# Performance work log

Hardware: AMD Instinct MI355X
Metric: run time of the kernel (lower is better)

Reference implementation:

```python
import jax, jax.numpy as jnp
import numpy as np

EPS_BN = 1e-5
EPS_LN = 1e-5


def conv2d(x, w, stride=1, padding=0):
    # x: [B,C,H,W], w: [O,I,kh,kw]
    return jax.lax.conv_general_dilated(
        x, w, (stride, stride), [(padding, padding), (padding, padding)],
        dimension_numbers=("NCHW", "OIHW", "NCHW"))


def bn_relu(x, g, b, m, v):
    inv = g / jnp.sqrt(v + EPS_BN)
    return jax.nn.relu(x * inv[None, :, None, None] + (b - m * inv)[None, :, None, None])


def haar_dwt(x):
    # orthonormal 2D Haar: [B,C,H,W] -> [B,4C,H/2,W/2] as concat(LL,LH,HL,HH)
    B, C, H, W = x.shape
    x = x.reshape(B, C, H // 2, 2, W // 2, 2)
    a = x[:, :, :, 0, :, 0]; b = x[:, :, :, 0, :, 1]
    c = x[:, :, :, 1, :, 0]; d = x[:, :, :, 1, :, 1]
    ll = (a + b + c + d) * 0.5
    lh = (a - b + c - d) * 0.5
    hl = (a + b - c - d) * 0.5
    hh = (a - b - c + d) * 0.5
    return jnp.concatenate([ll, lh, hl, hh], axis=1)


def haar_idwt(co):
    # exact inverse of haar_dwt: [B,4C,h,w] -> [B,C,2h,2w]
    B, C4, h, w = co.shape
    ll, lh, hl, hh = jnp.split(co, 4, axis=1)
    a = (ll + lh + hl + hh) * 0.5
    b = (ll - lh + hl - hh) * 0.5
    c = (ll + lh - hl - hh) * 0.5
    d = (ll - lh - hl + hh) * 0.5
    row0 = jnp.stack([a, b], axis=-1)  # [B,C,h,w,2]
    row1 = jnp.stack([c, d], axis=-1)
    y = jnp.stack([row0, row1], axis=3)  # [B,C,h,2,w,2]
    return y.reshape(B, C4 // 4, 2 * h, 2 * w)


def layernorm(x, g, b):
    mu = jnp.mean(x, axis=-1, keepdims=True)
    var = jnp.mean(jnp.square(x - mu), axis=-1, keepdims=True)
    return (x - mu) * jax.lax.rsqrt(var + EPS_LN) * g + b


def setup_inputs() -> dict:
    key = jax.random.key(0)
    ks = jax.random.split(key, 20)
    B, N, C = 16, 3136, 256
    red = C // 4  # 64
    sr = 2
    d = {}
    d["x"] = jax.random.normal(ks[0], (B, N, C), jnp.float32)
    d["height"] = 56
    d["width"] = 56
    # reduce: conv1x1 C->red (no bias) + BN
    d["reduce_w"] = jax.random.normal(ks[1], (red, C, 1, 1), jnp.float32) * 0.05
    d["bn1_g"] = jax.random.uniform(ks[2], (red,), jnp.float32, 0.5, 1.5)
    d["bn1_b"] = jax.random.normal(ks[3], (red,), jnp.float32) * 0.1
    d["bn1_m"] = jax.random.normal(ks[4], (red,), jnp.float32) * 0.1
    d["bn1_v"] = jax.random.uniform(ks[5], (red,), jnp.float32, 0.5, 1.5)
    # filter: conv3x3 C->C (no bias) + BN  (acts on 4*red = C coeff channels)
    d["filt_w"] = jax.random.normal(ks[6], (C, C, 3, 3), jnp.float32) * 0.02
    d["bn2_g"] = jax.random.uniform(ks[7], (C,), jnp.float32, 0.5, 1.5)
    d["bn2_b"] = jax.random.normal(ks[8], (C,), jnp.float32) * 0.1
    d["bn2_m"] = jax.random.normal(ks[9], (C,), jnp.float32) * 0.1
    d["bn2_v"] = jax.random.uniform(ks[10], (C,), jnp.float32, 0.5, 1.5)
    # kv_embed: conv kxk stride sr, C->C, with bias
    d["kve_w"] = jax.random.normal(ks[11], (C, C, sr, sr), jnp.float32) * 0.05
    d["kve_b"] = jnp.zeros((C,), jnp.float32)
    # q linear
    d["q_w"] = jax.random.normal(ks[12], (C, C), jnp.float32) * 0.05
    d["q_b"] = jnp.zeros((C,), jnp.float32)
    # kv layernorm + kv linear
    d["kvn_g"] = jnp.ones((C,), jnp.float32)
    d["kvn_b"] = jnp.zeros((C,), jnp.float32)
    d["kv_w"] = jax.random.normal(ks[13], (2 * C, C), jnp.float32) * 0.05
    d["kv_b"] = jnp.zeros((2 * C,), jnp.float32)
    # proj: (C + red) -> C
    d["proj_w"] = jax.random.normal(ks[14], (C, C + red), jnp.float32) * 0.05
    d["proj_b"] = jnp.zeros((C,), jnp.float32)
    return d


def reference(x, q_w, q_b, reduce_w, bn1_g, bn1_b, bn1_m, bn1_v,
              filt_w, bn2_g, bn2_b, bn2_m, bn2_v, kve_w, kve_b,
              kvn_g, kvn_b, kv_w, kv_b, proj_w, proj_b, height, width):
    B, N, C = x.shape
    H_heads, sr = 8, 2
    hd = C // H_heads
    scale = hd ** -0.5

    # queries [B,h,N,hd]
    q = (x @ q_w.T + q_b).reshape(B, N, H_heads, hd).transpose(0, 2, 1, 3)

    # spatial path
    spatial = x.transpose(0, 2, 1).reshape(B, C, height, width)
    reduced = bn_relu(conv2d(spatial, reduce_w), bn1_g, bn1_b, bn1_m, bn1_v)  # [B,C/4,H,W]
    coeffs = haar_dwt(reduced)  # [B,C,H/2,W/2]
    coeffs = bn_relu(conv2d(coeffs, filt_w, padding=1), bn2_g, bn2_b, bn2_m, bn2_v)
    local_context = haar_idwt(coeffs)  # [B,C/4,H,W]
    local_context = local_context.reshape(B, C // 4, N).transpose(0, 2, 1)  # [B,N,C/4]

    # kv path
    kv_src = conv2d(coeffs, kve_w, stride=sr) + kve_b[None, :, None, None]
    Bk, Ck, hk, wk = kv_src.shape
    kv_src = kv_src.reshape(B, C, hk * wk).transpose(0, 2, 1)  # [B,M,C]
    kv_src = layernorm(kv_src, kvn_g, kvn_b)
    kv = (kv_src @ kv_w.T + kv_b).reshape(B, -1, 2, H_heads, hd)
    kv = kv.transpose(2, 0, 3, 1, 4)  # [2,B,h,M,hd]
    key, value = kv[0], kv[1]

    # attention
    scores = jnp.einsum("bhnd,bhmd->bhnm", q, key) * scale
    probs = jax.nn.softmax(scores, axis=-1)
    attended = jnp.einsum("bhnm,bhmd->bhnd", probs, value)
    attended = attended.transpose(0, 2, 1, 3).reshape(B, N, C)

    out = jnp.concatenate([attended, local_context], axis=-1) @ proj_w.T + proj_b
    return out
```

## Files before the change

kernel.cpp:

```cpp
#include <hip/hip_runtime.h>
#include <hip/hip_bf16.h>
#include <math.h>


#define B_   16
#define NSP  3136
#define KVL  196
#define HD   32

typedef short bf16x8 __attribute__((ext_vector_type(8)));
typedef float f32x4  __attribute__((ext_vector_type(4)));

__device__ inline unsigned int f2bf(float f) {
    unsigned int u = __float_as_uint(f);
    u += 0x7FFFu + ((u >> 16) & 1u);
    return u >> 16;
}
__device__ inline float bf2f(unsigned short u) {
    return __uint_as_float(((unsigned int)u) << 16);
}
__device__ inline f32x4 max4(f32x4 a, f32x4 b) {
    f32x4 r;
    r[0] = fmaxf(a[0], b[0]); r[1] = fmaxf(a[1], b[1]);
    r[2] = fmaxf(a[2], b[2]); r[3] = fmaxf(a[3], b[3]);
    return r;
}
__device__ inline f32x4 add4(f32x4 a, f32x4 b) {
    f32x4 r;
    r[0] = a[0] + b[0]; r[1] = a[1] + b[1];
    r[2] = a[2] + b[2]; r[3] = a[3] + b[3];
    return r;
}

__global__ __launch_bounds__(256) void wcvt_k(
    const float* __restrict__ q, const float* __restrict__ red,
    const float* __restrict__ kv, const float* __restrict__ proj,
    unsigned short* __restrict__ dst)
{
    const int i = blockIdx.x * 256 + threadIdx.x;
    const int e = i * 4;
    const float* src; int off;
    if (e < 65536)       { src = q;    off = e; }
    else if (e < 81920)  { src = red;  off = e - 65536; }
    else if (e < 212992) { src = kv;   off = e - 81920; }
    else                 { src = proj; off = e - 212992; }
    const float4 v = *(const float4*)(src + off);
    const unsigned int p0 = f2bf(v.x) | (f2bf(v.y) << 16);
    const unsigned int p1 = f2bf(v.z) | (f2bf(v.w) << 16);
    *(uint2*)(dst + e) = make_uint2(p0, p1);
}

__global__ __launch_bounds__(256) void wcvt2_k(const float* __restrict__ kve,
                                               unsigned short* __restrict__ wk)
{
    const int i = blockIdx.x * 256 + threadIdx.x;
    const int n = i >> 8;
    const int rem = i & 255;
    const int tap = rem >> 6;
    const int ci0 = (rem & 63) * 4;
    const float* s = kve + (size_t)n * 1024;
    const unsigned int t0 = f2bf(s[(ci0 + 0) * 4 + tap]);
    const unsigned int t1 = f2bf(s[(ci0 + 1) * 4 + tap]);
    const unsigned int t2 = f2bf(s[(ci0 + 2) * 4 + tap]);
    const unsigned int t3 = f2bf(s[(ci0 + 3) * 4 + tap]);
    *(uint2*)(wk + (size_t)n * 1024 + tap * 256 + ci0) =
        make_uint2(t0 | (t1 << 16), t2 | (t3 << 16));
}

__global__ __launch_bounds__(256) void wcvt3_k(const float* __restrict__ filt,
                                               unsigned short* __restrict__ wf)
{
    const int i = blockIdx.x * 256 + threadIdx.x;
    const int n = i / 576;
    const int rem = (i - n * 576) * 4;
    const int tap = rem >> 8;
    const int ci = rem & 255;
    const float* s = filt + (size_t)n * 2304;
    const unsigned int t0 = f2bf(s[(ci + 0) * 9 + tap]);
    const unsigned int t1 = f2bf(s[(ci + 1) * 9 + tap]);
    const unsigned int t2 = f2bf(s[(ci + 2) * 9 + tap]);
    const unsigned int t3 = f2bf(s[(ci + 3) * 9 + tap]);
    *(uint2*)(wf + (size_t)n * 2304 + rem) = make_uint2(t0 | (t1 << 16), t2 | (t3 << 16));
}

template<int BM, int BN, int EPI, int LDM>
__global__ __launch_bounds__(256) void mgemm(
    const unsigned short* __restrict__ A, const float* __restrict__ Af,
    const unsigned short* __restrict__ Acl,
    const unsigned short* __restrict__ W, const float* __restrict__ bias,
    const float* __restrict__ g, const float* __restrict__ bb,
    const float* __restrict__ mm, const float* __restrict__ vv,
    float* __restrict__ out, float* __restrict__ out2,
    int Mpad, int Mvalid, int N, int K, float scale)
{
    constexpr int FM = BM / 32, FN = BN / 32;
    constexpr int RA = BM / 64, RB = BN / 64;
    __shared__ short As[BM][32];
    __shared__ short Bs[BN][32];
    const int tid = threadIdx.x, lane = tid & 63;
    const int w = tid >> 6, wr = w >> 1, wc = w & 1;
    const int b = blockIdx.z, m0 = blockIdx.x * BM, n0 = blockIdx.y * BN;
    const unsigned short* Ab = A + ((size_t)b * Mpad + m0) * (size_t)K;
    const unsigned short* Wb = W + (size_t)n0 * K;

    const int r_row0 = tid >> 2, kbase = (tid & 3) * 8;
    int ym[RA], xm[RA], mg[RA];
#pragma unroll
    for (int rnd = 0; rnd < RA; ++rnd) {
        const int m = m0 + rnd * 64 + r_row0;
        mg[rnd] = m;
        if constexpr (LDM == 1) { ym[rnd] = m / 28; xm[rnd] = m - 28 * ym[rnd]; }
        else if constexpr (LDM == 3) { ym[rnd] = m / 14; xm[rnd] = m - 14 * ym[rnd]; }
        else { ym[rnd] = 0; xm[rnd] = 0; }
    }

    f32x4 acc[FM][FN];
#pragma unroll
    for (int i = 0; i < FM; ++i)
#pragma unroll
        for (int j = 0; j < FN; ++j) acc[i][j] = (f32x4){0.f, 0.f, 0.f, 0.f};

    for (int k0 = 0; k0 < K; k0 += 32) {
#pragma unroll
        for (int rnd = 0; rnd < RA; ++rnd) {
            const int row = rnd * 64 + r_row0;
            if constexpr (LDM == 0) {
                *(int4*)&As[row][kbase] =
                    *(const int4*)(Ab + (size_t)row * K + k0 + kbase);
            } else if constexpr (LDM == 2) {
                unsigned int p0 = 0, p1 = 0, p2 = 0, p3 = 0;
                if (mg[rnd] < Mvalid) {
                    const float* sp = Af + ((size_t)b * Mvalid + mg[rnd]) * K + k0 + kbase;
                    const float4 v0 = *(const float4*)sp;
                    const float4 v1 = *(const float4*)(sp + 4);
                    p0 = f2bf(v0.x) | (f2bf(v0.y) << 16);
                    p1 = f2bf(v0.z) | (f2bf(v0.w) << 16);
                    p2 = f2bf(v1.x) | (f2bf(v1.y) << 16);
                    p3 = f2bf(v1.z) | (f2bf(v1.w) << 16);
                }
                *(int4*)&As[row][kbase] = make_int4(p0, p1, p2, p3);
            } else if constexpr (LDM == 1) {
                const int kk = k0 + kbase;
                const int tap = kk >> 8, ci0 = kk & 255;
                const int ky = tap / 3, kx = tap - 3 * ky;
                const int sy = ym[rnd] + ky - 1, sx = xm[rnd] + kx - 1;
                int4 v = make_int4(0, 0, 0, 0);
                if (mg[rnd] < Mvalid && sy >= 0 && sy < 28 && sx >= 0 && sx < 28)
                    v = *(const int4*)(Acl + ((size_t)b * 784 + sy * 28 + sx) * 256 + ci0);
                *(int4*)&As[row][kbase] = v;
            } else {
                const int kk = k0 + kbase;
                const int tap = kk >> 8, ci0 = kk & 255;
                const int ky = tap >> 1, kx = tap & 1;
                const int sy = 2 * ym[rnd] + ky, sx = 2 * xm[rnd] + kx;
                int4 v = make_int4(0, 0, 0, 0);
                if (mg[rnd] < Mvalid)
                    v = *(const int4*)(Acl + ((size_t)b * 784 + sy * 28 + sx) * 256 + ci0);
                *(int4*)&As[row][kbase] = v;
            }
        }
#pragma unroll
        for (int rnd = 0; rnd < RB; ++rnd) {
            const int row = rnd * 64 + r_row0;
            *(int4*)&Bs[row][kbase] =
                *(const int4*)(Wb + (size_t)row * K + k0 + kbase);
        }
        __syncthreads();
        bf16x8 af[FM], bfr[FN];
#pragma unroll
        for (int i = 0; i < FM; ++i)
            af[i] = *(const bf16x8*)&As[wr * (BM / 2) + i * 16 + (lane & 15)][(lane >> 4) * 8];
#pragma unroll
        for (int j = 0; j < FN; ++j)
            bfr[j] = *(const bf16x8*)&Bs[wc * (BN / 2) + j * 16 + (lane & 15)][(lane >> 4) * 8];
#pragma unroll
        for (int i = 0; i < FM; ++i)
#pragma unroll
            for (int j = 0; j < FN; ++j)
                acc[i][j] = __builtin_amdgcn_mfma_f32_16x16x32_bf16(af[i], bfr[j], acc[i][j], 0, 0, 0);
        __syncthreads();
    }

    const int cl = lane & 15, rh = lane >> 4;
#pragma unroll
    for (int i = 0; i < FM; ++i) {
#pragma unroll
        for (int j = 0; j < FN; ++j) {
            const int n = n0 + wc * (BN / 2) + j * 16 + cl;
#pragma unroll
            for (int r = 0; r < 4; ++r) {
                const int m = m0 + wr * (BM / 2) + i * 16 + rh * 4 + r;
                if (m >= Mvalid) continue;
                const float v = acc[i][j][r];
                if constexpr (EPI == 0) {
                    out[((size_t)b * Mvalid + m) * N + n] = v + bias[n];
                } else if constexpr (EPI == 1) {
                    unsigned short* qp = (unsigned short*)out;
                    const int h = (n >> 5) & 7, d = n & 31;
                    qp[(((size_t)b * 8 + h) * 3136 + m) * 32 + d] =
                        (unsigned short)f2bf((v + bias[n]) * scale);
                } else if constexpr (EPI == 3) {
                    const float val = v + bias[n];
                    const int h = (n >> 5) & 7, d = n & 31;
                    if (n < 256)
                        ((unsigned short*)out)[(((size_t)b * 8 + h) * 224 + m) * 32 + d] =
                            (unsigned short)f2bf(val);
                    else
                        ((unsigned short*)out2)[(((size_t)b * 8 + h) * 32 + d) * 224 + m] =
                            (unsigned short)f2bf(val);
                } else {
                    const float inv = g[n] * rsqrtf(vv[n] + 1e-5f);
                    const float rr = v * inv + (bb[n] - mm[n] * inv);
                    ((unsigned short*)out)[((size_t)b * Mvalid + m) * N + n] =
                        (unsigned short)f2bf(rr > 0.f ? rr : 0.f);
                }
            }
        }
    }
}

__global__ __launch_bounds__(256) void dwt_k(const unsigned short* __restrict__ rd,
                                             unsigned short* __restrict__ ccl)
{
    const int i = blockIdx.x * 256 + threadIdx.x;
    const int c4 = (i & 15) * 4;
    const int p = i >> 4;
    const int x = p % 28, y = (p / 28) % 28, b = p / 784;
    const unsigned short* ip = rd + ((size_t)b * 3136 + (2 * y) * 56 + 2 * x) * 64 + c4;
    const uint2 u00 = *(const uint2*)(ip);
    const uint2 u01 = *(const uint2*)(ip + 64);
    const uint2 u10 = *(const uint2*)(ip + 56 * 64);
    const uint2 u11 = *(const uint2*)(ip + 57 * 64);
    const unsigned short* s00 = (const unsigned short*)&u00;
    const unsigned short* s01 = (const unsigned short*)&u01;
    const unsigned short* s10 = (const unsigned short*)&u10;
    const unsigned short* s11 = (const unsigned short*)&u11;
    unsigned short ll[4], lh[4], hl[4], hh[4];
#pragma unroll
    for (int j = 0; j < 4; ++j) {
        const float a = bf2f(s00[j]), bq = bf2f(s01[j]);
        const float c = bf2f(s10[j]), d = bf2f(s11[j]);
        ll[j] = (unsigned short)f2bf((a + bq + c + d) * 0.5f);
        lh[j] = (unsigned short)f2bf((a - bq + c - d) * 0.5f);
        hl[j] = (unsigned short)f2bf((a + bq - c - d) * 0.5f);
        hh[j] = (unsigned short)f2bf((a - bq - c + d) * 0.5f);
    }
    unsigned short* op = ccl + ((size_t)b * 784 + y * 28 + x) * 256 + c4;
    *(uint2*)(op)       = make_uint2(ll[0] | (ll[1] << 16), ll[2] | (ll[3] << 16));
    *(uint2*)(op + 64)  = make_uint2(lh[0] | (lh[1] << 16), lh[2] | (lh[3] << 16));
    *(uint2*)(op + 128) = make_uint2(hl[0] | (hl[1] << 16), hl[2] | (hl[3] << 16));
    *(uint2*)(op + 192) = make_uint2(hh[0] | (hh[1] << 16), hh[2] | (hh[3] << 16));
}

__global__ __launch_bounds__(256) void idwt_k(const unsigned short* __restrict__ c2,
                                              unsigned short* __restrict__ aproj)
{
    const int i = blockIdx.x * 256 + threadIdx.x;
    const int c4 = (i & 15) * 4;
    const int p = i >> 4;
    const int m = p % 3136, b = p / 3136;
    const int Y = m / 56, X = m - 56 * Y;
    const int y = Y >> 1, x = X >> 1;
    const unsigned short* ip = c2 + ((size_t)b * 784 + y * 28 + x) * 256 + c4;
    const uint2 ull = *(const uint2*)(ip);
    const uint2 ulh = *(const uint2*)(ip + 64);
    const uint2 uhl = *(const uint2*)(ip + 128);
    const uint2 uhh = *(const uint2*)(ip + 192);
    const unsigned short* sll = (const unsigned short*)&ull;
    const unsigned short* slh = (const unsigned short*)&ulh;
    const unsigned short* shl = (const unsigned short*)&uhl;
    const unsigned short* shh = (const unsigned short*)&uhh;
    const float flh = (X & 1) ? -0.5f : 0.5f;
    const float fhl = (Y & 1) ? -0.5f : 0.5f;
    const float fhh = ((X ^ Y) & 1) ? -0.5f : 0.5f;
    unsigned short o[4];
#pragma unroll
    for (int j = 0; j < 4; ++j) {
        const float v = 0.5f * bf2f(sll[j]) + flh * bf2f(slh[j]) +
                        fhl * bf2f(shl[j]) + fhh * bf2f(shh[j]);
        o[j] = (unsigned short)f2bf(v);
    }
    *(uint2*)(aproj + ((size_t)b * 3200 + m) * 320 + 256 + c4) =
        make_uint2(o[0] | (o[1] << 16), o[2] | (o[3] << 16));
}

__global__ __launch_bounds__(256) void ln_k(const float* __restrict__ in,
                                            const float* __restrict__ g,
                                            const float* __restrict__ bb,
                                            unsigned short* __restrict__ outp)
{
    const int rg = blockIdx.x;
    const int rl = rg & 255, b = rg >> 8;
    const int t = threadIdx.x;
    unsigned short* op = outp + (size_t)rg * 256 + t;
    if (rl >= 196) { *op = 0; return; }
    const float x = in[((size_t)(b * 196) + rl) * 256 + t];
    __shared__ float r1[4], r2[4];
    float s = x;
#pragma unroll
    for (int o = 32; o > 0; o >>= 1) s += __shfl_down(s, o);
    if ((t & 63) == 0) r1[t >> 6] = s;
    __syncthreads();
    const float mu = (r1[0] + r1[1] + r1[2] + r1[3]) * (1.f / 256.f);
    const float d = x - mu;
    float s2 = d * d;
#pragma unroll
    for (int o = 32; o > 0; o >>= 1) s2 += __shfl_down(s2, o);
    if ((t & 63) == 0) r2[t >> 6] = s2;
    __syncthreads();
    const float var = (r2[0] + r2[1] + r2[2] + r2[3]) * (1.f / 256.f);
    *op = (unsigned short)f2bf(d * rsqrtf(var + 1e-5f) * g[t] + bb[t]);
}

__global__ __launch_bounds__(256) void attn_m(
    const unsigned short* __restrict__ qb, const unsigned short* __restrict__ kb,
    const unsigned short* __restrict__ vt, unsigned short* __restrict__ aproj)
{
    __shared__ short Pl[4][16][232];
    const int tid = threadIdx.x, lane = tid & 63, w = tid >> 6;
    const int bh = blockIdx.y, b = bh >> 3, h = bh & 7;
    const int q0 = blockIdx.x * 64 + w * 16;
    const int cl = lane & 15, hi = lane >> 4;

    const bf16x8 qf = *(const bf16x8*)(qb + ((size_t)bh * 3136 + q0 + cl) * 32 + hi * 8);

    f32x4 s[13];
    const unsigned short* kp = kb + (size_t)bh * 224 * 32;
#pragma unroll
    for (int t = 0; t < 13; ++t) {
        const bf16x8 kf = *(const bf16x8*)(kp + (size_t)(t * 16 + cl) * 32 + hi * 8);
        s[t] = __builtin_amdgcn_mfma_f32_16x16x32_bf16(kf, qf,
                                                       (f32x4){0.f, 0.f, 0.f, 0.f}, 0, 0, 0);
    }
    if (hi) s[12] = (f32x4){-1e30f, -1e30f, -1e30f, -1e30f};

    f32x4 t0 = max4(s[0], s[1]), t1 = max4(s[2], s[3]), t2 = max4(s[4], s[5]);
    f32x4 t3 = max4(s[6], s[7]), t4 = max4(s[8], s[9]), t5 = max4(s[10], s[11]);
    t0 = max4(t0, t1); t2 = max4(t2, t3); t4 = max4(t4, s[12]);
    t0 = max4(t0, t2); t0 = max4(t0, max4(t4, t5));
    float m = fmaxf(fmaxf(t0[0], t0[1]), fmaxf(t0[2], t0[3]));
    m = fmaxf(m, __shfl_xor(m, 16));
    m = fmaxf(m, __shfl_xor(m, 32));

#pragma unroll
    for (int t = 0; t < 13; ++t) {
#pragma unroll
        for (int r = 0; r < 4; ++r) s[t][r] = exp2f(s[t][r] - m);
    }
    f32x4 a0 = add4(s[0], s[1]), a1 = add4(s[2], s[3]), a2 = add4(s[4], s[5]);
    f32x4 a3 = add4(s[6], s[7]), a4 = add4(s[8], s[9]), a5 = add4(s[10], s[11]);
    a0 = add4(a0, a1); a2 = add4(a2, a3); a4 = add4(a4, s[12]);
    a0 = add4(a0, a2); a0 = add4(a0, add4(a4, a5));
    float l = (a0[0] + a0[1]) + (a0[2] + a0[3]);
    l += __shfl_xor(l, 16);
    l += __shfl_xor(l, 32);
    const float rl = 1.f / l;

    short* prow = &Pl[w][cl][0];
#pragma unroll
    for (int t = 0; t < 13; ++t) {
        __hip_bfloat162 pa = __float22bfloat162_rn(make_float2(s[t][0], s[t][1]));
        __hip_bfloat162 pb = __float22bfloat162_rn(make_float2(s[t][2], s[t][3]));
        unsigned int ua, ub;
        __builtin_memcpy(&ua, &pa, 4);
        __builtin_memcpy(&ub, &pb, 4);
        *(uint2*)(prow + t * 16 + hi * 4) = make_uint2(ua, ub);
    }
    *(uint2*)(prow + 208 + hi * 4) = make_uint2(0u, 0u);

    f32x4 o0 = (f32x4){0.f, 0.f, 0.f, 0.f};
    f32x4 o1 = (f32x4){0.f, 0.f, 0.f, 0.f};
    const unsigned short* vp0 = vt + ((size_t)bh * 32 + cl) * 224;
    const unsigned short* vp1 = vp0 + 16 * 224;
#pragma unroll
    for (int kk = 0; kk < 7; ++kk) {
        const bf16x8 pf = *(const bf16x8*)(prow + kk * 32 + hi * 8);
        const bf16x8 v0 = *(const bf16x8*)(vp0 + kk * 32 + hi * 8);
        const bf16x8 v1 = *(const bf16x8*)(vp1 + kk * 32 + hi * 8);
        o0 = __builtin_amdgcn_mfma_f32_16x16x32_bf16(pf, v0, o0, 0, 0, 0);
        o1 = __builtin_amdgcn_mfma_f32_16x16x32_bf16(pf, v1, o1, 0, 0, 0);
    }

    float* ol = (float*)&Pl[w][0][0];
#pragma unroll
    for (int r = 0; r < 4; ++r) {
        const float rlq = __shfl(rl, hi * 4 + r);
        ol[(hi * 4 + r) * 36 + cl]      = o0[r] * rlq;
        ol[(hi * 4 + r) * 36 + cl + 16] = o1[r] * rlq;
    }
    const int row = lane >> 2, c8 = (lane & 3) * 8;
    const float4 b0 = *(const float4*)(ol + row * 36 + c8);
    const float4 b1 = *(const float4*)(ol + row * 36 + c8 + 4);
    const unsigned int k0 = f2bf(b0.x) | (f2bf(b0.y) << 16);
    const unsigned int k1 = f2bf(b0.z) | (f2bf(b0.w) << 16);
    const unsigned int k2 = f2bf(b1.x) | (f2bf(b1.y) << 16);
    const unsigned int k3 = f2bf(b1.z) | (f2bf(b1.w) << 16);
    *(uint4*)(aproj + ((size_t)b * 3200 + q0 + row) * 320 + h * 32 + c8) =
        make_uint4(k0, k1, k2, k3);
}

extern "C" void kernel_launch(void* const* d_in, const int* in_sizes, int n_in,
                              void* d_out, int out_size, void* d_ws, size_t ws_size,
                              hipStream_t stream)
{
    const float* x        = (const float*)d_in[0];
    const float* reduce_w = (const float*)d_in[3];
    const float* bn1_g    = (const float*)d_in[4];
    const float* bn1_b    = (const float*)d_in[5];
    const float* bn1_m    = (const float*)d_in[6];
    const float* bn1_v    = (const float*)d_in[7];
    const float* filt_w   = (const float*)d_in[8];
    const float* bn2_g    = (const float*)d_in[9];
    const float* bn2_b    = (const float*)d_in[10];
    const float* bn2_m    = (const float*)d_in[11];
    const float* bn2_v    = (const float*)d_in[12];
    const float* kve_w    = (const float*)d_in[13];
    const float* kve_b    = (const float*)d_in[14];
    const float* q_w      = (const float*)d_in[15];
    const float* q_b      = (const float*)d_in[16];
    const float* kvn_g    = (const float*)d_in[17];
    const float* kvn_b    = (const float*)d_in[18];
    const float* kv_w     = (const float*)d_in[19];
    const float* kv_b     = (const float*)d_in[20];
    const float* proj_w   = (const float*)d_in[21];
    const float* proj_b   = (const float*)d_in[22];

    float* out = (float*)d_out;
    float* ws  = (float*)d_ws;

    unsigned short* aproj = (unsigned short*)ws;
    unsigned short* rd_cl = (unsigned short*)(ws +  8192000);
    unsigned short* ccl   = (unsigned short*)(ws +  9797632);
    unsigned short* ccl2  = (unsigned short*)(ws + 11403264);
    float* kv_src         = ws + 13008896;
    unsigned short* kbuf  = (unsigned short*)(ws + 13811712);
    unsigned short* vtb   = (unsigned short*)(ws + 14270464);
    unsigned short* kv_ln = (unsigned short*)(ws + 14729216);
    unsigned short* wpl   = (unsigned short*)(ws + 15253504);
    unsigned short* wkve  = (unsigned short*)(ws + 15400960);
    unsigned short* wfilt = (unsigned short*)(ws + 15532032);
    unsigned short* wq    = wpl;
    unsigned short* wred  = wpl + 65536;
    unsigned short* wkv   = wpl + 81920;
    unsigned short* wproj = wpl + 212992;
    unsigned short* qb    = (unsigned short*)d_out;

    const float scale = 0.17677669529663689f * 1.4426950408889634f;

    wcvt_k<<<288, 256, 0, stream>>>(q_w, reduce_w, kv_w, proj_w, wpl);
    wcvt2_k<<<256, 256, 0, stream>>>(kve_w, wkve);
    wcvt3_k<<<576, 256, 0, stream>>>(filt_w, wfilt);

    mgemm<128, 128, 1, 2><<<dim3(25, 2, B_), 256, 0, stream>>>(
        nullptr, x, nullptr, wq, q_b, nullptr, nullptr, nullptr, nullptr,
        out, nullptr, 3136, 3136, 256, 256, scale);

    mgemm<128, 64, 4, 2><<<dim3(25, 1, B_), 256, 0, stream>>>(
        nullptr, x, nullptr, wred, nullptr, bn1_g, bn1_b, bn1_m, bn1_v,
        (float*)rd_cl, nullptr, 3136, 3136, 64, 256, 0.f);

    dwt_k<<<784, 256, 0, stream>>>(rd_cl, ccl);

    mgemm<64, 64, 4, 1><<<dim3(13, 4, B_), 256, 0, stream>>>(
        nullptr, nullptr, ccl, wfilt, nullptr, bn2_g, bn2_b, bn2_m, bn2_v,
        (float*)ccl2, nullptr, 832, 784, 256, 2304, 0.f);

    idwt_k<<<3136, 256, 0, stream>>>(ccl2, aproj);

    mgemm<64, 64, 0, 3><<<dim3(4, 4, B_), 256, 0, stream>>>(
        nullptr, nullptr, ccl2, wkve, kve_b, nullptr, nullptr, nullptr, nullptr,
        kv_src, nullptr, 256, 196, 256, 1024, 0.f);

    ln_k<<<4096, 256, 0, stream>>>(kv_src, kvn_g, kvn_b, kv_ln);

    mgemm<64, 128, 3, 0><<<dim3(4, 4, B_), 256, 0, stream>>>(
        kv_ln, nullptr, nullptr, wkv, kv_b, nullptr, nullptr, nullptr, nullptr,
        (float*)kbuf, (float*)vtb, 256, 196, 512, 256, 0.f);

    attn_m<<<dim3(49, 128), 256, 0, stream>>>(qb, kbuf, vtb, aproj);

    mgemm<128, 128, 0, 0><<<dim3(25, 2, B_), 256, 0, stream>>>(
        aproj, nullptr, nullptr, wproj, proj_b, nullptr, nullptr, nullptr, nullptr,
        out, nullptr, 3200, 3136, 256, 320, 0.f);
}
```

Baseline: 263.5 us.

## Fuse Q projection and reduce conv into one GEMM; compute softmax sum via MFMA

The Q projection GEMM and the 1x1 reduce conv GEMM both read x with K=256, and they are merged into a single GEMM with N=320 over the concatenated bf16 weights. A new epilogue sends columns below 256 to the scaled Q layout and the remaining columns through BN+ReLU into the reduced buffer. This way x is loaded and converted once instead of twice. In the attention kernel, the softmax denominator now comes from an extra MFMA against a ones vector instead of a shuffle reduction, and the output bf16 packing uses the intrinsic conversion. The fused GEMM uses a 64x320 tile, which changes occupancy and register pressure, and the row sum is now taken over bf16-rounded probabilities.

Measured after the change: 294.3 us. 1.12x slower.

```diff
diff --git a/kernel.cpp b/kernel.cpp
--- a/kernel.cpp
+++ b/kernel.cpp
@@ -23,12 +23,6 @@
     f32x4 r;
     r[0] = fmaxf(a[0], b[0]); r[1] = fmaxf(a[1], b[1]);
     r[2] = fmaxf(a[2], b[2]); r[3] = fmaxf(a[3], b[3]);
-    return r;
-}
-__device__ inline f32x4 add4(f32x4 a, f32x4 b) {
-    f32x4 r;
-    r[0] = a[0] + b[0]; r[1] = a[1] + b[1];
-    r[2] = a[2] + b[2]; r[3] = a[3] + b[3];
     return r;
 }
 
@@ -194,11 +188,6 @@
                 const float v = acc[i][j][r];
                 if constexpr (EPI == 0) {
                     out[((size_t)b * Mvalid + m) * N + n] = v + bias[n];
-                } else if constexpr (EPI == 1) {
-                    unsigned short* qp = (unsigned short*)out;
-                    const int h = (n >> 5) & 7, d = n & 31;
-                    qp[(((size_t)b * 8 + h) * 3136 + m) * 32 + d] =
-                        (unsigned short)f2bf((v + bias[n]) * scale);
                 } else if constexpr (EPI == 3) {
                     const float val = v + bias[n];
                     const int h = (n >> 5) & 7, d = n & 31;
@@ -208,11 +197,24 @@
                     else
                         ((unsigned short*)out2)[(((size_t)b * 8 + h) * 32 + d) * 224 + m] =
                             (unsigned short)f2bf(val);
-                } else {
+                } else if constexpr (EPI == 4) {
                     const float inv = g[n] * rsqrtf(vv[n] + 1e-5f);
                     const float rr = v * inv + (bb[n] - mm[n] * inv);
                     ((unsigned short*)out)[((size_t)b * Mvalid + m) * N + n] =
                         (unsigned short)f2bf(rr > 0.f ? rr : 0.f);
+                } else {
+                    if (n < 256) {
+                        unsigned short* qp = (unsigned short*)out;
+                        const int h = n >> 5, d = n & 31;
+                        qp[(((size_t)b * 8 + h) * 3136 + m) * 32 + d] =
+                            (unsigned short)f2bf((v + bias[n]) * scale);
+                    } else {
+                        const int c = n - 256;
+                        const float inv = g[c] * rsqrtf(vv[c] + 1e-5f);
+                        const float rr = v * inv + (bb[c] - mm[c] * inv);
+                        ((unsigned short*)out2)[((size_t)b * 3136 + m) * 64 + c] =
+                            (unsigned short)f2bf(rr > 0.f ? rr : 0.f);
+                    }
                 }
             }
         }
@@ -347,14 +349,6 @@
 #pragma unroll
         for (int r = 0; r < 4; ++r) s[t][r] = exp2f(s[t][r] - m);
     }
-    f32x4 a0 = add4(s[0], s[1]), a1 = add4(s[2], s[3]), a2 = add4(s[4], s[5]);
-    f32x4 a3 = add4(s[6], s[7]), a4 = add4(s[8], s[9]), a5 = add4(s[10], s[11]);
-    a0 = add4(a0, a1); a2 = add4(a2, a3); a4 = add4(a4, s[12]);
-    a0 = add4(a0, a2); a0 = add4(a0, add4(a4, a5));
-    float l = (a0[0] + a0[1]) + (a0[2] + a0[3]);
-    l += __shfl_xor(l, 16);
-    l += __shfl_xor(l, 32);
-    const float rl = 1.f / l;
 
     short* prow = &Pl[w][cl][0];
 #pragma unroll
@@ -368,8 +362,12 @@
     }
     *(uint2*)(prow + 208 + hi * 4) = make_uint2(0u, 0u);
 
+    bf16x8 onesf;
+#pragma unroll
+    for (int j = 0; j < 8; ++j) onesf[j] = (short)0x3F80;
     f32x4 o0 = (f32x4){0.f, 0.f, 0.f, 0.f};
     f32x4 o1 = (f32x4){0.f, 0.f, 0.f, 0.f};
+    f32x4 osum = (f32x4){0.f, 0.f, 0.f, 0.f};
     const unsigned short* vp0 = vt + ((size_t)bh * 32 + cl) * 224;
     const unsigned short* vp1 = vp0 + 16 * 224;
 #pragma unroll
@@ -379,22 +377,28 @@
         const bf16x8 v1 = *(const bf16x8*)(vp1 + kk * 32 + hi * 8);
         o0 = __builtin_amdgcn_mfma_f32_16x16x32_bf16(pf, v0, o0, 0, 0, 0);
         o1 = __builtin_amdgcn_mfma_f32_16x16x32_bf16(pf, v1, o1, 0, 0, 0);
+        osum = __builtin_amdgcn_mfma_f32_16x16x32_bf16(pf, onesf, osum, 0, 0, 0);
     }
 
     float* ol = (float*)&Pl[w][0][0];
 #pragma unroll
     for (int r = 0; r < 4; ++r) {
-        const float rlq = __shfl(rl, hi * 4 + r);
-        ol[(hi * 4 + r) * 36 + cl]      = o0[r] * rlq;
-        ol[(hi * 4 + r) * 36 + cl + 16] = o1[r] * rlq;
+        const float rq = __builtin_amdgcn_rcpf(osum[r]);
+        ol[(hi * 4 + r) * 36 + cl]      = o0[r] * rq;
+        ol[(hi * 4 + r) * 36 + cl + 16] = o1[r] * rq;
     }
     const int row = lane >> 2, c8 = (lane & 3) * 8;
     const float4 b0 = *(const float4*)(ol + row * 36 + c8);
     const float4 b1 = *(const float4*)(ol + row * 36 + c8 + 4);
-    const unsigned int k0 = f2bf(b0.x) | (f2bf(b0.y) << 16);
-    const unsigned int k1 = f2bf(b0.z) | (f2bf(b0.w) << 16);
-    const unsigned int k2 = f2bf(b1.x) | (f2bf(b1.y) << 16);
-    const unsigned int k3 = f2bf(b1.z) | (f2bf(b1.w) << 16);
+    __hip_bfloat162 pa = __float22bfloat162_rn(make_float2(b0.x, b0.y));
+    __hip_bfloat162 pb = __float22bfloat162_rn(make_float2(b0.z, b0.w));
+    __hip_bfloat162 pc = __float22bfloat162_rn(make_float2(b1.x, b1.y));
+    __hip_bfloat162 pd = __float22bfloat162_rn(make_float2(b1.z, b1.w));
+    unsigned int k0, k1, k2, k3;
+    __builtin_memcpy(&k0, &pa, 4);
+    __builtin_memcpy(&k1, &pb, 4);
+    __builtin_memcpy(&k2, &pc, 4);
+    __builtin_memcpy(&k3, &pd, 4);
     *(uint4*)(aproj + ((size_t)b * 3200 + q0 + row) * 320 + h * 32 + c8) =
         make_uint4(k0, k1, k2, k3);
 }
@@ -439,8 +443,6 @@
     unsigned short* wpl   = (unsigned short*)(ws + 15253504);
     unsigned short* wkve  = (unsigned short*)(ws + 15400960);
     unsigned short* wfilt = (unsigned short*)(ws + 15532032);
-    unsigned short* wq    = wpl;
-    unsigned short* wred  = wpl + 65536;
     unsigned short* wkv   = wpl + 81920;
     unsigned short* wproj = wpl + 212992;
     unsigned short* qb    = (unsigned short*)d_out;
@@ -451,13 +453,9 @@
     wcvt2_k<<<256, 256, 0, stream>>>(kve_w, wkve);
     wcvt3_k<<<576, 256, 0, stream>>>(filt_w, wfilt);
 
-    mgemm<128, 128, 1, 2><<<dim3(25, 2, B_), 256, 0, stream>>>(
-        nullptr, x, nullptr, wq, q_b, nullptr, nullptr, nullptr, nullptr,
-        out, nullptr, 3136, 3136, 256, 256, scale);
-
-    mgemm<128, 64, 4, 2><<<dim3(25, 1, B_), 256, 0, stream>>>(
-        nullptr, x, nullptr, wred, nullptr, bn1_g, bn1_b, bn1_m, bn1_v,
-        (float*)rd_cl, nullptr, 3136, 3136, 64, 256, 0.f);
+    mgemm<64, 320, 5, 2><<<dim3(49, 1, B_), 256, 0, stream>>>(
+        nullptr, x, nullptr, wpl, q_b, bn1_g, bn1_b, bn1_m, bn1_v,
+        out, (float*)rd_cl, 3136, 3136, 320, 256, scale);
 
     dwt_k<<<784, 256, 0, stream>>>(rd_cl, ccl);
 
```
